# Kernel optimization log

Hardware: AMD Instinct MI355X
Metric: run time of the kernel (lower is better)

Reference implementation:

```python
import jax, jax.numpy as jnp
import numpy as np

REG_MAX = 16
BOX_W = 7.5
OBJ_W = 1.0
TOPK = 10
EPS = 1e-7


def dfl_decode(x, reg_max):
    # x: [B, 4*reg_max, N] -> expected value of per-side distribution -> [B, N, 4] (xyxy)
    B, C, N = x.shape
    x = x.reshape(B, 4, reg_max, N)
    p = jax.nn.softmax(x, axis=2)
    proj = jnp.arange(reg_max, dtype=x.dtype)
    return jnp.einsum('bkrn,r->bnk', p, proj)


def bbox_ciou(b1, b2):
    # b1: [B,N,1,4], b2: [B,1,M,4], xyxy -> [B,N,M]
    x11, y11, x12, y12 = b1[..., 0], b1[..., 1], b1[..., 2], b1[..., 3]
    x21, y21, x22, y22 = b2[..., 0], b2[..., 1], b2[..., 2], b2[..., 3]
    w1, h1 = x12 - x11, y12 - y11
    w2, h2 = x22 - x21, y22 - y21
    iw = jnp.clip(jnp.minimum(x12, x22) - jnp.maximum(x11, x21), 0.0)
    ih = jnp.clip(jnp.minimum(y12, y22) - jnp.maximum(y11, y21), 0.0)
    inter = iw * ih
    union = w1 * h1 + w2 * h2 - inter + EPS
    iou = inter / union
    cw = jnp.maximum(x12, x22) - jnp.minimum(x11, x21)
    ch = jnp.maximum(y12, y22) - jnp.minimum(y11, y21)
    c2 = cw * cw + ch * ch + EPS
    rho2 = ((x21 + x22 - x11 - x12) ** 2 + (y21 + y22 - y11 - y12) ** 2) * 0.25
    v = (4.0 / (np.pi ** 2)) * (jnp.arctan(w2 / (h2 + EPS)) - jnp.arctan(w1 / (h1 + EPS))) ** 2
    alpha = jax.lax.stop_gradient(v / (v - iou + 1.0 + EPS))
    return iou - rho2 / c2 - alpha * v


def setup_inputs() -> dict:
    key = jax.random.key(0)
    k1, k2, k3, k4 = jax.random.split(key, 4)
    B, N, M = 8, 34000, 64
    boxes = jax.random.normal(k1, (B, 4 * REG_MAX, N), dtype=jnp.float32)
    scores = jax.random.normal(k2, (B, N), dtype=jnp.float32)
    # GT boxes: valid xyxy in roughly the same [0, reg_max) range as decoded preds
    xy = jax.random.uniform(k3, (B, M, 2), dtype=jnp.float32) * 11.0
    wh = jax.random.uniform(k4, (B, M, 2), dtype=jnp.float32) * 4.0 + 0.5
    targets = jnp.concatenate([xy, xy + wh], axis=-1)
    return {'boxes': boxes, 'scores': scores, 'targets': targets}


def reference(boxes, scores, targets):
    B, N = scores.shape
    M = targets.shape[1]
    pb = dfl_decode(boxes, REG_MAX)                     # [B,N,4]
    ciou = bbox_ciou(pb[:, :, None, :], targets[:, None, :, :])  # [B,N,M]
    k = min(TOPK, N)
    topv, topi = jax.lax.top_k(jnp.swapaxes(ciou, 1, 2), k)      # [B,M,k] over anchors
    valid = topv > 0.0
    vals = jnp.where(valid, topv, 0.0)

    def per_batch(idx, val, vld):
        flat_i = idx.reshape(-1)
        iou_t = jnp.zeros((N,), val.dtype).at[flat_i].max(val.reshape(-1))
        pos = jnp.zeros((N,), bool).at[flat_i].max(vld.reshape(-1))
        return iou_t, pos

    iou_target, pos = jax.vmap(per_batch)(topi, vals, valid)     # [B,N]
    posf = pos.astype(iou_target.dtype)
    npos = posf.sum(axis=1)
    box_per = jnp.where(npos > 0,
                        ((1.0 - iou_target) * posf).sum(axis=1) / jnp.maximum(npos, 1.0),
                        0.0)
    box_loss = box_per.sum()
    # BCEWithLogits (mean over anchors), summed over batch
    bce = jnp.maximum(scores, 0.0) - scores * iou_target + jnp.log1p(jnp.exp(-jnp.abs(scores)))
    obj_loss = bce.mean(axis=1).sum()
    total = (BOX_W * box_loss + OBJ_W * obj_loss) / B
    return total, box_loss, obj_loss
```

## Files before the change

kernel.cpp:

```cpp
#include <hip/hip_runtime.h>
#include <math.h>

#define BQ 8
#define MQ 64
#define REGMAX 16
#define KTOP 10
#define EPSQ 1e-7f
#define APB 1024
#define MBUF 1024

__device__ __forceinline__ float frcp(float x) { return __builtin_amdgcn_rcpf(x); }

__device__ __forceinline__ float dfl_side(const float* __restrict__ p, size_t Ns) {
  float x0 = p[0];
  float x1 = p[Ns];
  float x2 = p[2 * Ns];
  float x3 = p[3 * Ns];
  float x4 = p[4 * Ns];
  float x5 = p[5 * Ns];
  float x6 = p[6 * Ns];
  float x7 = p[7 * Ns];
  float x8 = p[8 * Ns];
  float x9 = p[9 * Ns];
  float x10 = p[10 * Ns];
  float x11 = p[11 * Ns];
  float x12 = p[12 * Ns];
  float x13 = p[13 * Ns];
  float x14 = p[14 * Ns];
  float x15 = p[15 * Ns];
  float mx = fmaxf(fmaxf(fmaxf(fmaxf(x0, x1), fmaxf(x2, x3)),
                         fmaxf(fmaxf(x4, x5), fmaxf(x6, x7))),
                   fmaxf(fmaxf(fmaxf(x8, x9), fmaxf(x10, x11)),
                         fmaxf(fmaxf(x12, x13), fmaxf(x14, x15))));
  float s = 0.f, ws = 0.f, e;
  e = __expf(x0 - mx); s += e;
  e = __expf(x1 - mx); s += e; ws += 1.f * e;
  e = __expf(x2 - mx); s += e; ws += 2.f * e;
  e = __expf(x3 - mx); s += e; ws += 3.f * e;
  e = __expf(x4 - mx); s += e; ws += 4.f * e;
  e = __expf(x5 - mx); s += e; ws += 5.f * e;
  e = __expf(x6 - mx); s += e; ws += 6.f * e;
  e = __expf(x7 - mx); s += e; ws += 7.f * e;
  e = __expf(x8 - mx); s += e; ws += 8.f * e;
  e = __expf(x9 - mx); s += e; ws += 9.f * e;
  e = __expf(x10 - mx); s += e; ws += 10.f * e;
  e = __expf(x11 - mx); s += e; ws += 11.f * e;
  e = __expf(x12 - mx); s += e; ws += 12.f * e;
  e = __expf(x13 - mx); s += e; ws += 13.f * e;
  e = __expf(x14 - mx); s += e; ws += 14.f * e;
  e = __expf(x15 - mx); s += e; ws += 15.f * e;
  return ws * frcp(s);
}

__device__ __forceinline__ float4 dfl_side4(const float* __restrict__ p, size_t Ns) {
  float4 x0 = *(const float4*)(p);
  float4 x1 = *(const float4*)(p + Ns);
  float4 x2 = *(const float4*)(p + 2 * Ns);
  float4 x3 = *(const float4*)(p + 3 * Ns);
  float4 x4 = *(const float4*)(p + 4 * Ns);
  float4 x5 = *(const float4*)(p + 5 * Ns);
  float4 x6 = *(const float4*)(p + 6 * Ns);
  float4 x7 = *(const float4*)(p + 7 * Ns);
  float4 x8 = *(const float4*)(p + 8 * Ns);
  float4 x9 = *(const float4*)(p + 9 * Ns);
  float4 x10 = *(const float4*)(p + 10 * Ns);
  float4 x11 = *(const float4*)(p + 11 * Ns);
  float4 x12 = *(const float4*)(p + 12 * Ns);
  float4 x13 = *(const float4*)(p + 13 * Ns);
  float4 x14 = *(const float4*)(p + 14 * Ns);
  float4 x15 = *(const float4*)(p + 15 * Ns);
#define MAX16(c)                                                        \
  fmaxf(fmaxf(fmaxf(fmaxf(x0.c, x1.c), fmaxf(x2.c, x3.c)),              \
              fmaxf(fmaxf(x4.c, x5.c), fmaxf(x6.c, x7.c))),             \
        fmaxf(fmaxf(fmaxf(x8.c, x9.c), fmaxf(x10.c, x11.c)),            \
              fmaxf(fmaxf(x12.c, x13.c), fmaxf(x14.c, x15.c))))
  float mxa = MAX16(x);
  float mxb = MAX16(y);
  float mxc = MAX16(z);
  float mxd = MAX16(w);
#undef MAX16
  float sa = 0.f, wa = 0.f, sb = 0.f, wb = 0.f;
  float sc = 0.f, wc = 0.f, sd = 0.f, wd = 0.f;
  float e;
#define STEP(K, XK)                                      \
  e = __expf(XK.x - mxa); sa += e; wa += (float)K * e;   \
  e = __expf(XK.y - mxb); sb += e; wb += (float)K * e;   \
  e = __expf(XK.z - mxc); sc += e; wc += (float)K * e;   \
  e = __expf(XK.w - mxd); sd += e; wd += (float)K * e;
  STEP(0, x0) STEP(1, x1) STEP(2, x2) STEP(3, x3)
  STEP(4, x4) STEP(5, x5) STEP(6, x6) STEP(7, x7)
  STEP(8, x8) STEP(9, x9) STEP(10, x10) STEP(11, x11)
  STEP(12, x12) STEP(13, x13) STEP(14, x14) STEP(15, x15)
#undef STEP
  return make_float4(wa * frcp(sa), wb * frcp(sb), wc * frcp(sc), wd * frcp(sd));
}

__global__ __launch_bounds__(256) void decode_topk_kernel(
    const float* __restrict__ boxes, const float* __restrict__ scores,
    const float* __restrict__ targets, unsigned int* __restrict__ iou_bits,
    uint2* __restrict__ cand, float* __restrict__ bcePartial,
    unsigned int* __restrict__ ctr, int N, int bpb) {
  const int tid = threadIdx.x;
  const int b = blockIdx.x / bpb;
  const int blk = blockIdx.x - b * bpb;
  const int a0 = blk * APB;
  const int w = tid >> 6;
  const int l = tid & 63;

  __shared__ float4 s_sv[APB];
  __shared__ float s_at[APB];
  __shared__ int s_ix[APB];
  __shared__ float s_hv[4 * MQ * KTOP];
  __shared__ int s_hi[4 * MQ * KTOP];
  __shared__ uint2 s_mg[MQ * KTOP];
  __shared__ int s_cnt;
  __shared__ float s_bce;
  if (tid == 0) { s_cnt = 0; s_bce = 0.f; }
  if (blockIdx.x == 0 && tid == 0) *ctr = 0u;
  __syncthreads();

  auto emit = [&](float e0, float e1, float e2, float e3, int n) {
    float w1 = e2 - e0, h1 = e3 - e1;
    if (w1 > 0.f && h1 > 0.f) {
      int slot = atomicAdd(&s_cnt, 1);
      s_sv[slot] = make_float4(e0, e1, e2, e3);
      s_at[slot] = atanf(w1 * frcp(h1 + EPSQ));
      s_ix[slot] = n;
    }
  };

  const int n0 = a0 + 4 * tid;
  float bce0 = 0.f;
  if (n0 < N) {
    const size_t i = (size_t)b * N + n0;
    const size_t Ns = (size_t)N;
    const float* base = boxes + (size_t)(b * 64) * Ns + n0;
    if ((N & 3) == 0 && n0 + 3 < N) {
      *(uint4*)(iou_bits + i) = make_uint4(0u, 0u, 0u, 0u);
      float4 sc4 = *(const float4*)(scores + i);
      bce0 = fmaxf(sc4.x, 0.f) + log1pf(__expf(-fabsf(sc4.x))) +
             fmaxf(sc4.y, 0.f) + log1pf(__expf(-fabsf(sc4.y))) +
             fmaxf(sc4.z, 0.f) + log1pf(__expf(-fabsf(sc4.z))) +
             fmaxf(sc4.w, 0.f) + log1pf(__expf(-fabsf(sc4.w)));
      float4 ev0 = dfl_side4(base, Ns);
      float4 ev1 = dfl_side4(base + 16 * Ns, Ns);
      float4 ev2 = dfl_side4(base + 32 * Ns, Ns);
      float4 ev3 = dfl_side4(base + 48 * Ns, Ns);
      emit(ev0.x, ev1.x, ev2.x, ev3.x, n0 + 0);
      emit(ev0.y, ev1.y, ev2.y, ev3.y, n0 + 1);
      emit(ev0.z, ev1.z, ev2.z, ev3.z, n0 + 2);
      emit(ev0.w, ev1.w, ev2.w, ev3.w, n0 + 3);
    } else {
      for (int k = 0; k < 4; ++k) {
        int n = n0 + k;
        if (n >= N) break;
        iou_bits[i + k] = 0u;
        float sc = scores[i + k];
        bce0 += fmaxf(sc, 0.f) + log1pf(__expf(-fabsf(sc)));
        const float* bp = base + k;
        float ev0 = dfl_side(bp, Ns);
        float ev1 = dfl_side(bp + 16 * Ns, Ns);
        float ev2 = dfl_side(bp + 32 * Ns, Ns);
        float ev3 = dfl_side(bp + 48 * Ns, Ns);
        emit(ev0, ev1, ev2, ev3, n);
      }
    }
  }
#pragma unroll
  for (int d = 1; d < 64; d <<= 1) bce0 += __shfl_xor(bce0, d, 64);
  if (l == 0) atomicAdd(&s_bce, bce0);
  __syncthreads();
  const int nsurv = s_cnt;
  if (tid == 0) bcePartial[blockIdx.x] = s_bce;

  const float4 t = ((const float4*)targets)[b * MQ + l];
  const float x21 = t.x, y21 = t.y, x22 = t.z, y22 = t.w;
  const float w2 = x22 - x21, h2 = y22 - y21;
  const float atan_t = atanf(w2 * frcp(h2 + EPSQ));
  const float area2 = w2 * h2, sumx2 = x21 + x22, sumy2 = y21 + y22;
  const float CPI = 4.0f / (float)(M_PI * M_PI);

  float hv0 = 0.f, hv1 = 0.f, hv2 = 0.f, hv3 = 0.f, hv4 = 0.f;
  float hv5 = 0.f, hv6 = 0.f, hv7 = 0.f, hv8 = 0.f, hv9 = 0.f;
  int hi0 = 0, hi1 = 0, hi2 = 0, hi3 = 0, hi4 = 0;
  int hi5 = 0, hi6 = 0, hi7 = 0, hi8 = 0, hi9 = 0;

  const int qlen = (nsurv + 3) >> 2;
  const int j0 = w * qlen;
  const int j1 = min(nsurv, j0 + qlen);
  for (int j = j0; j < j1; ++j) {
    float4 p = s_sv[j];
    float pa = s_at[j];
    int ixj = s_ix[j];
    float x11 = p.x, y11 = p.y, x12 = p.z, y12 = p.w;
    float w1 = x12 - x11, h1 = y12 - y11;
    float iw = fmaxf(fminf(x12, x22) - fmaxf(x11, x21), 0.f);
    float ih = fmaxf(fminf(y12, y22) - fmaxf(y11, y21), 0.f);
    float inter = iw * ih;
    float uni = w1 * h1 + area2 - inter + EPSQ;
    float iou = inter * frcp(uni);
    float cw = fmaxf(x12, x22) - fminf(x11, x21);
    float ch = fmaxf(y12, y22) - fminf(y11, y21);
    float c2 = cw * cw + ch * ch + EPSQ;
    float dx = sumx2 - x11 - x12;
    float dy = sumy2 - y11 - y12;
    float rho2 = (dx * dx + dy * dy) * 0.25f;
    float da = atan_t - pa;
    float v = CPI * da * da;
    float alpha = v * frcp(v - iou + 1.f + EPSQ);
    float ciou = iou - rho2 * frcp(c2) - alpha * v;
    if (ciou > hv9) {
      float cv = ciou;
      int ci = ixj;
#define INS(vk, ik)                         \
  {                                         \
    bool gt = cv > vk;                      \
    float tv_ = vk; int ti_ = ik;           \
    vk = gt ? cv : vk; ik = gt ? ci : ik;   \
    cv = gt ? tv_ : cv; ci = gt ? ti_ : ci; \
  }
      INS(hv0, hi0) INS(hv1, hi1) INS(hv2, hi2) INS(hv3, hi3) INS(hv4, hi4)
      INS(hv5, hi5) INS(hv6, hi6) INS(hv7, hi7) INS(hv8, hi8) INS(hv9, hi9)
#undef INS
    }
  }
  const int hb = (w * MQ + l) * KTOP;
  s_hv[hb + 0] = hv0; s_hi[hb + 0] = hi0;
  s_hv[hb + 1] = hv1; s_hi[hb + 1] = hi1;
  s_hv[hb + 2] = hv2; s_hi[hb + 2] = hi2;
  s_hv[hb + 3] = hv3; s_hi[hb + 3] = hi3;
  s_hv[hb + 4] = hv4; s_hi[hb + 4] = hi4;
  s_hv[hb + 5] = hv5; s_hi[hb + 5] = hi5;
  s_hv[hb + 6] = hv6; s_hi[hb + 6] = hi6;
  s_hv[hb + 7] = hv7; s_hi[hb + 7] = hi7;
  s_hv[hb + 8] = hv8; s_hi[hb + 8] = hi8;
  s_hv[hb + 9] = hv9; s_hi[hb + 9] = hi9;
  __syncthreads();

  if (w == 0) {
    const int m = l;
    int p0 = 0, p1 = 0, p2 = 0, p3 = 0;
    for (int r = 0; r < KTOP; ++r) {
      float c0 = s_hv[(0 * MQ + m) * KTOP + p0];
      float c1 = s_hv[(1 * MQ + m) * KTOP + p1];
      float c2m = s_hv[(2 * MQ + m) * KTOP + p2];
      float c3 = s_hv[(3 * MQ + m) * KTOP + p3];
      float best = c0; int bw = 0;
      if (c1 > best) { best = c1; bw = 1; }
      if (c2m > best) { best = c2m; bw = 2; }
      if (c3 > best) { best = c3; bw = 3; }
      int psel = (bw == 0) ? p0 : (bw == 1) ? p1 : (bw == 2) ? p2 : p3;
      int bidx = s_hi[(bw * MQ + m) * KTOP + psel];
      s_mg[m * KTOP + r] = make_uint2(__float_as_uint(best), (unsigned)bidx);
      if (bw == 0) p0 = min(p0 + 1, KTOP - 1);
      else if (bw == 1) p1 = min(p1 + 1, KTOP - 1);
      else if (bw == 2) p2 = min(p2 + 1, KTOP - 1);
      else p3 = min(p3 + 1, KTOP - 1);
    }
  }
  __syncthreads();
  for (int sl = tid; sl < MQ * KTOP; sl += 256) {
    int m = sl / KTOP;
    int r = sl - m * KTOP;
    cand[((size_t)(b * MQ + m) * bpb + blk) * KTOP + r] = s_mg[sl];
  }
}

__device__ __forceinline__ void select_top10(
    float* s_bv, int* s_bi, float* s_winv, int* s_wini,
    int* s_cnt, int c, int tid) {
  if (tid < 64) {
    for (int r = 0; r < KTOP; ++r) {
      float bv = 0.f;
      int bs = 0xffff;
      for (int sl = tid; sl < c; sl += 64) {
        float v = s_bv[sl];
        if (v > bv) { bv = v; bs = sl; }
      }
      unsigned long long key =
          ((unsigned long long)__float_as_uint(bv) << 32) | (unsigned int)bs;
#pragma unroll
      for (int d = 1; d < 64; d <<= 1) {
        unsigned long long o = __shfl_xor(key, d, 64);
        if (o > key) key = o;
      }
      if (tid == 0) {
        float wv = __uint_as_float((unsigned int)(key >> 32));
        int ws = (int)(key & 0xffffu);
        s_winv[r] = wv;
        if (wv > 0.f && ws != 0xffff) {
          s_wini[r] = s_bi[ws];
          s_bv[ws] = 0.f;
        } else {
          s_wini[r] = 0;
        }
      }
    }
    if (tid < KTOP) { s_bv[tid] = s_winv[tid]; s_bi[tid] = s_wini[tid]; }
    if (tid == 0) *s_cnt = KTOP;
  }
}

__global__ __launch_bounds__(256) void merge_kernel(
    const uint2* __restrict__ cand, const float* __restrict__ scores,
    unsigned int* __restrict__ iou_bits, const float* __restrict__ bcePartial,
    float* __restrict__ mergePartial, unsigned int* __restrict__ ctr,
    float* __restrict__ out, int N, int bpb) {
  const int bm = blockIdx.x;
  const int b = bm >> 6;
  const int tid = threadIdx.x;
  const int NC = bpb * KTOP;

  __shared__ float s_bv[MBUF];
  __shared__ int s_bi[MBUF];
  __shared__ float s_winv[KTOP];
  __shared__ int s_wini[KTOP];
  __shared__ int s_cnt;
  __shared__ float s_d[3];
  __shared__ int s_last;
  __shared__ float s_acc[BQ * 3];
  if (tid == 0) s_cnt = 0;
  if (tid < 3) s_d[tid] = 0.f;
  if (tid < BQ * 3) s_acc[tid] = 0.f;
  __syncthreads();

  const uint2* cbase = cand + (size_t)bm * NC;
  for (int k2 = tid; k2 < NC; k2 += 256) {
    uint2 e = cbase[k2];
    float v = __uint_as_float(e.x);
    if (v > 0.f) {
      int slot = atomicAdd(&s_cnt, 1);
      s_bv[slot] = v;
      s_bi[slot] = (int)e.y;
    }
  }
  __syncthreads();
  int c = s_cnt;
  __syncthreads();
  if (c > KTOP) {
    select_top10(s_bv, s_bi, s_winv, s_wini, &s_cnt, c, tid);
    __syncthreads();
    c = KTOP;
  }
  if (tid < KTOP && tid < c) {
    float v = s_bv[tid];
    if (v > 0.f) {
      int ix = s_bi[tid];
      unsigned int vb = __float_as_uint(v);
      unsigned int old = atomicMax(&iou_bits[(size_t)b * N + ix], vb);
      if (old < vb) {
        float vold = __uint_as_float(old);
        bool was = (old != 0u);
        atomicAdd(&s_d[0], was ? (vold - v) : (1.f - v));
        if (!was) atomicAdd(&s_d[1], 1.f);
        atomicAdd(&s_d[2], -scores[(size_t)b * N + ix] * (v - vold));
      }
    }
  }
  __syncthreads();
  if (tid == 0) {
    float4* mp = (float4*)(mergePartial + (size_t)bm * 4);
    *mp = make_float4(s_d[0], s_d[1], s_d[2], 0.f);
    __threadfence();
    unsigned int done = atomicAdd(ctr, 1u);
    s_last = (done == (unsigned)(gridDim.x - 1)) ? 1 : 0;
  }
  __syncthreads();
  if (s_last) {
    __threadfence();
    volatile const float* mp = mergePartial;
    for (int i = tid; i < BQ * MQ; i += 256) {
      int bb = i >> 6;
      float a0 = mp[i * 4 + 0];
      float a1 = mp[i * 4 + 1];
      float a2 = mp[i * 4 + 2];
      atomicAdd(&s_acc[bb * 3 + 0], a0);
      atomicAdd(&s_acc[bb * 3 + 1], a1);
      atomicAdd(&s_acc[bb * 3 + 2], a2);
    }
    volatile const float* bp = bcePartial;
    for (int i = tid; i < BQ * bpb; i += 256) {
      int bb = i / bpb;
      atomicAdd(&s_acc[bb * 3 + 2], bp[i]);
    }
    __syncthreads();
    if (tid == 0) {
      float box = 0.f, obj = 0.f;
      for (int bb = 0; bb < BQ; ++bb) {
        float np = s_acc[bb * 3 + 1];
        box += (np > 0.f) ? s_acc[bb * 3 + 0] / fmaxf(np, 1.f) : 0.f;
        obj += s_acc[bb * 3 + 2] / (float)N;
      }
      out[0] = (7.5f * box + obj) / (float)BQ;
      out[1] = box;
      out[2] = obj;
    }
  }
}

extern "C" void kernel_launch(void* const* d_in, const int* in_sizes, int n_in,
                              void* d_out, int out_size, void* d_ws, size_t ws_size,
                              hipStream_t stream) {
  const float* boxes = (const float*)d_in[0];
  const float* scores = (const float*)d_in[1];
  const float* targets = (const float*)d_in[2];
  float* out = (float*)d_out;
  const int N = in_sizes[1] / BQ;

  const int bpb = (N + APB - 1) / APB;
  const int nblk = BQ * bpb;

  char* ws = (char*)d_ws;
  size_t cand_bytes = (size_t)BQ * MQ * bpb * KTOP * sizeof(uint2);
  size_t iou_bytes = (size_t)BQ * N * sizeof(unsigned int);
  size_t bce_bytes = (((size_t)nblk * sizeof(float)) + 255) & ~(size_t)255;
  size_t mp_bytes = (size_t)BQ * MQ * 4 * sizeof(float);

  uint2* cand = (uint2*)ws;                    ws += cand_bytes;
  unsigned int* iou_bits = (unsigned int*)ws;  ws += iou_bytes;
  float* bcePartial = (float*)ws;              ws += bce_bytes;
  float* mergePartial = (float*)ws;            ws += mp_bytes;
  unsigned int* ctr = (unsigned int*)ws;

  decode_topk_kernel<<<nblk, 256, 0, stream>>>(boxes, scores, targets,
                                               iou_bits, cand, bcePartial, ctr, N, bpb);
  merge_kernel<<<BQ * MQ, 256, 0, stream>>>(cand, scores, iou_bits, bcePartial,
                                            mergePartial, ctr, out, N, bpb);
}
```

Before: 159.3 us.

## Shrink anchors per block to one per thread and use wave-aggregated compaction

```diff
diff --git a/kernel.cpp b/kernel.cpp
--- a/kernel.cpp
+++ b/kernel.cpp
@@ -6,8 +6,8 @@
 #define REGMAX 16
 #define KTOP 10
 #define EPSQ 1e-7f
-#define APB 1024
-#define MBUF 1024
+#define APB 256
+#define MBUF 1344
 
 __device__ __forceinline__ float frcp(float x) { return __builtin_amdgcn_rcpf(x); }
 
@@ -52,50 +52,7 @@
   return ws * frcp(s);
 }
 
-__device__ __forceinline__ float4 dfl_side4(const float* __restrict__ p, size_t Ns) {
-  float4 x0 = *(const float4*)(p);
-  float4 x1 = *(const float4*)(p + Ns);
-  float4 x2 = *(const float4*)(p + 2 * Ns);
-  float4 x3 = *(const float4*)(p + 3 * Ns);
-  float4 x4 = *(const float4*)(p + 4 * Ns);
-  float4 x5 = *(const float4*)(p + 5 * Ns);
-  float4 x6 = *(const float4*)(p + 6 * Ns);
-  float4 x7 = *(const float4*)(p + 7 * Ns);
-  float4 x8 = *(const float4*)(p + 8 * Ns);
-  float4 x9 = *(const float4*)(p + 9 * Ns);
-  float4 x10 = *(const float4*)(p + 10 * Ns);
-  float4 x11 = *(const float4*)(p + 11 * Ns);
-  float4 x12 = *(const float4*)(p + 12 * Ns);
-  float4 x13 = *(const float4*)(p + 13 * Ns);
-  float4 x14 = *(const float4*)(p + 14 * Ns);
-  float4 x15 = *(const float4*)(p + 15 * Ns);
-#define MAX16(c)                                                        \
-  fmaxf(fmaxf(fmaxf(fmaxf(x0.c, x1.c), fmaxf(x2.c, x3.c)),              \
-              fmaxf(fmaxf(x4.c, x5.c), fmaxf(x6.c, x7.c))),             \
-        fmaxf(fmaxf(fmaxf(x8.c, x9.c), fmaxf(x10.c, x11.c)),            \
-              fmaxf(fmaxf(x12.c, x13.c), fmaxf(x14.c, x15.c))))
-  float mxa = MAX16(x);
-  float mxb = MAX16(y);
-  float mxc = MAX16(z);
-  float mxd = MAX16(w);
-#undef MAX16
-  float sa = 0.f, wa = 0.f, sb = 0.f, wb = 0.f;
-  float sc = 0.f, wc = 0.f, sd = 0.f, wd = 0.f;
-  float e;
-#define STEP(K, XK)                                      \
-  e = __expf(XK.x - mxa); sa += e; wa += (float)K * e;   \
-  e = __expf(XK.y - mxb); sb += e; wb += (float)K * e;   \
-  e = __expf(XK.z - mxc); sc += e; wc += (float)K * e;   \
-  e = __expf(XK.w - mxd); sd += e; wd += (float)K * e;
-  STEP(0, x0) STEP(1, x1) STEP(2, x2) STEP(3, x3)
-  STEP(4, x4) STEP(5, x5) STEP(6, x6) STEP(7, x7)
-  STEP(8, x8) STEP(9, x9) STEP(10, x10) STEP(11, x11)
-  STEP(12, x12) STEP(13, x13) STEP(14, x14) STEP(15, x15)
-#undef STEP
-  return make_float4(wa * frcp(sa), wb * frcp(sb), wc * frcp(sc), wd * frcp(sd));
-}
-
-__global__ __launch_bounds__(256) void decode_topk_kernel(
+__global__ __launch_bounds__(256, 4) void decode_topk_kernel(
     const float* __restrict__ boxes, const float* __restrict__ scores,
     const float* __restrict__ targets, unsigned int* __restrict__ iou_bits,
     uint2* __restrict__ cand, float* __restrict__ bcePartial,
@@ -119,51 +76,38 @@
   if (blockIdx.x == 0 && tid == 0) *ctr = 0u;
   __syncthreads();
 
-  auto emit = [&](float e0, float e1, float e2, float e3, int n) {
+  const int n = a0 + tid;
+  float bce0 = 0.f;
+  bool pred = false;
+  float e0 = 0.f, e1 = 0.f, e2 = 0.f, e3 = 0.f, at = 0.f;
+  if (n < N) {
+    const size_t i = (size_t)b * N + n;
+    iou_bits[i] = 0u;
+    float sc = scores[i];
+    bce0 = fmaxf(sc, 0.f) + log1pf(__expf(-fabsf(sc)));
+    const size_t Ns = (size_t)N;
+    const float* base = boxes + (size_t)(b * 64) * Ns + n;
+    e0 = dfl_side(base, Ns);
+    e1 = dfl_side(base + 16 * Ns, Ns);
+    e2 = dfl_side(base + 32 * Ns, Ns);
+    e3 = dfl_side(base + 48 * Ns, Ns);
     float w1 = e2 - e0, h1 = e3 - e1;
     if (w1 > 0.f && h1 > 0.f) {
-      int slot = atomicAdd(&s_cnt, 1);
-      s_sv[slot] = make_float4(e0, e1, e2, e3);
-      s_at[slot] = atanf(w1 * frcp(h1 + EPSQ));
-      s_ix[slot] = n;
-    }
-  };
-
-  const int n0 = a0 + 4 * tid;
-  float bce0 = 0.f;
-  if (n0 < N) {
-    const size_t i = (size_t)b * N + n0;
-    const size_t Ns = (size_t)N;
-    const float* base = boxes + (size_t)(b * 64) * Ns + n0;
-    if ((N & 3) == 0 && n0 + 3 < N) {
-      *(uint4*)(iou_bits + i) = make_uint4(0u, 0u, 0u, 0u);
-      float4 sc4 = *(const float4*)(scores + i);
-      bce0 = fmaxf(sc4.x, 0.f) + log1pf(__expf(-fabsf(sc4.x))) +
-             fmaxf(sc4.y, 0.f) + log1pf(__expf(-fabsf(sc4.y))) +
-             fmaxf(sc4.z, 0.f) + log1pf(__expf(-fabsf(sc4.z))) +
-             fmaxf(sc4.w, 0.f) + log1pf(__expf(-fabsf(sc4.w)));
-      float4 ev0 = dfl_side4(base, Ns);
-      float4 ev1 = dfl_side4(base + 16 * Ns, Ns);
-      float4 ev2 = dfl_side4(base + 32 * Ns, Ns);
-      float4 ev3 = dfl_side4(base + 48 * Ns, Ns);
-      emit(ev0.x, ev1.x, ev2.x, ev3.x, n0 + 0);
-      emit(ev0.y, ev1.y, ev2.y, ev3.y, n0 + 1);
-      emit(ev0.z, ev1.z, ev2.z, ev3.z, n0 + 2);
-      emit(ev0.w, ev1.w, ev2.w, ev3.w, n0 + 3);
-    } else {
-      for (int k = 0; k < 4; ++k) {
-        int n = n0 + k;
-        if (n >= N) break;
-        iou_bits[i + k] = 0u;
-        float sc = scores[i + k];
-        bce0 += fmaxf(sc, 0.f) + log1pf(__expf(-fabsf(sc)));
-        const float* bp = base + k;
-        float ev0 = dfl_side(bp, Ns);
-        float ev1 = dfl_side(bp + 16 * Ns, Ns);
-        float ev2 = dfl_side(bp + 32 * Ns, Ns);
-        float ev3 = dfl_side(bp + 48 * Ns, Ns);
-        emit(ev0, ev1, ev2, ev3, n);
-      }
+      pred = true;
+      at = atanf(w1 * frcp(h1 + EPSQ));
+    }
+  }
+  {
+    unsigned long long mask = __ballot(pred);
+    int cnt = __popcll(mask);
+    int bslot = 0;
+    if (l == 0 && cnt) bslot = atomicAdd(&s_cnt, cnt);
+    bslot = __shfl(bslot, 0, 64);
+    if (pred) {
+      int pos = bslot + __popcll(mask & ((1ull << l) - 1ull));
+      s_sv[pos] = make_float4(e0, e1, e2, e3);
+      s_at[pos] = at;
+      s_ix[pos] = n;
     }
   }
 #pragma unroll
@@ -309,6 +253,7 @@
   const int bm = blockIdx.x;
   const int b = bm >> 6;
   const int tid = threadIdx.x;
+  const int l = tid & 63;
   const int NC = bpb * KTOP;
 
   __shared__ float s_bv[MBUF];
@@ -328,10 +273,16 @@
   for (int k2 = tid; k2 < NC; k2 += 256) {
     uint2 e = cbase[k2];
     float v = __uint_as_float(e.x);
-    if (v > 0.f) {
-      int slot = atomicAdd(&s_cnt, 1);
-      s_bv[slot] = v;
-      s_bi[slot] = (int)e.y;
+    bool p = v > 0.f;
+    unsigned long long mask = __ballot(p);
+    int cnt = __popcll(mask);
+    int bslot = 0;
+    if (l == 0 && cnt) bslot = atomicAdd(&s_cnt, cnt);
+    bslot = __shfl(bslot, 0, 64);
+    if (p) {
+      int pos = bslot + __popcll(mask & ((1ull << l) - 1ull));
+      s_bv[pos] = v;
+      s_bi[pos] = (int)e.y;
     }
   }
   __syncthreads();
```

Result: faster. 143.8 us (-9.7%).
